# Kernel tuning notes

Hardware: AMD Instinct MI355X
Metric: run time of the kernel (lower is better)

## Reference

```python
import jax, jax.numpy as jnp
import numpy as np

B, R, C, OUT, IN = 256, 1152, 10, 16, 8


def setup_inputs() -> dict:
    key = jax.random.key(0)
    kx, kw = jax.random.split(key)
    x = jax.random.normal(kx, (B, R, IN), dtype=jnp.float32)
    W = jax.random.normal(kw, (R, C, OUT, IN), dtype=jnp.float32)
    return {"x": x, "W": W}


def _squash(s):
    # s: [B, C, OUT]
    mag_sq = jnp.sum(s * s, axis=-1, keepdims=True)
    mag = jnp.sqrt(mag_sq + 1e-8)
    return mag_sq / (1.0 + mag_sq) * (s / (mag + 1e-8))


def reference(x, W):
    # u_hat[b,r,c,o] = sum_i W[r,c,o,i] * x[b,r,i]  (no explicit W.repeat)
    u_hat = jnp.einsum('rcoi,bri->brco', W, x)
    b_ij = jnp.zeros((B, R, C), dtype=u_hat.dtype)
    v_j = None
    for it in range(3):
        c_ij = jax.nn.softmax(b_ij, axis=2)              # [B,R,C]
        s_j = jnp.einsum('brc,brco->bco', c_ij, u_hat)   # [B,C,OUT]
        v_j = _squash(s_j)                               # [B,C,OUT]
        if it < 2:
            b_ij = b_ij + jnp.einsum('brco,bco->brc', u_hat, v_j)
    return v_j
```

## Files before the change

kernel.cpp:

```cpp
#include <hip/hip_runtime.h>
#include <math.h>


typedef _Float16 h2 __attribute__((ext_vector_type(2)));
typedef _Float16 h4 __attribute__((ext_vector_type(4)));

#if __has_builtin(__builtin_amdgcn_fdot2)
#define FDOT2(a, b, c) __builtin_amdgcn_fdot2((a), (b), (c), false)
#else
static __device__ __forceinline__ float FDOT2(h2 a, h2 b, float c) {
    return c + (float)a.x * (float)b.x + (float)a.y * (float)b.y;
}
#endif

#if __has_builtin(__builtin_amdgcn_rcpf)
#define FRCP(x) __builtin_amdgcn_rcpf(x)
#else
#define FRCP(x) (1.0f / (x))
#endif

#define BCH2(u) __builtin_bit_cast(h2, (u))

template<int CTRL>
static __device__ __forceinline__ float dpp_xadd(float x) {
    const int t = __builtin_amdgcn_update_dpp(
        0, __builtin_bit_cast(int, x), CTRL, 0xF, 0xF, true);
    return x + __builtin_bit_cast(float, t);
}
static __device__ __forceinline__ float og_allsum(float l) {
    l = dpp_xadd<0xB1>(l);
    l = dpp_xadd<0x4E>(l);
    l = dpp_xadd<0x141>(l);
    return l;
}

namespace {
constexpr int Bdim = 256;
constexpr int Rdim = 1152;
constexpr int Cdim = 10;
constexpr int Odim = 16;
constexpr int Idim = 8;
constexpr int CO   = 160;

constexpr int Rpad  = 1280;
constexpr int RPC   = 10;
constexpr int NPAIR = 5;
constexpr int NSP   = 32;
constexpr int WROW  = Cdim * Odim * Idim;
}

__global__ __launch_bounds__(256)
void conv_wx(const float* __restrict__ W, const float* __restrict__ x,
             _Float16* __restrict__ W16, _Float16* __restrict__ X16)
{
    constexpr int NW4 = Rpad * WROW / 4;
    constexpr int NX4 = Rpad * Bdim * Idim / 4;
    const int i = blockIdx.x * 256 + threadIdx.x;
    if (i < NW4) {
        const int r = i / (WROW / 4);
        h4 o = { (_Float16)0.f, (_Float16)0.f, (_Float16)0.f, (_Float16)0.f };
        if (r < Rdim) {
            const float4 v = reinterpret_cast<const float4*>(W)[i];
            o = { (_Float16)v.x, (_Float16)v.y, (_Float16)v.z, (_Float16)v.w };
        }
        reinterpret_cast<h4*>(W16)[i] = o;
    } else if (i < NW4 + NX4) {
        const int j    = i - NW4;
        const int r    = j / (Bdim * 2);
        const int rem  = j - r * (Bdim * 2);
        const int b    = rem >> 1;
        const int half = rem & 1;
        h4 o = { (_Float16)0.f, (_Float16)0.f, (_Float16)0.f, (_Float16)0.f };
        if (r < Rdim) {
            const float4 v = reinterpret_cast<const float4*>(x)
                [((size_t)b * Rdim + r) * 2 + half];
            o = { (_Float16)v.x, (_Float16)v.y, (_Float16)v.z, (_Float16)v.w };
        }
        reinterpret_cast<h4*>(X16)[j] = o;
    }
}

__device__ __forceinline__ void stagepair(const _Float16* __restrict__ src,
                                          _Float16* dst, int lane)
{
#pragma unroll
    for (int k = 0; k < 5; ++k) {
        const _Float16* s = src + (size_t)(k * 64 + lane) * 8;
        _Float16* d = dst + k * 512;
        __builtin_amdgcn_global_load_lds((const __attribute__((address_space(1))) void*)s,
                                         (__attribute__((address_space(3))) void*)d,
                                         16, 0, 0);
    }
}

template<bool FIRST>
__global__ __launch_bounds__(256)
void caps_iter(const _Float16* __restrict__ X16, const _Float16* __restrict__ W16,
               const float* __restrict__ Vsum, float* __restrict__ s_part)
{
    __shared__ __align__(16) _Float16 Wst[4][3][2560];

    const int tid  = threadIdx.x;
    const int wv   = tid >> 6;
    const int lane = tid & 63;
    const int og   = lane & 7;
    const int bl   = lane >> 3;

    const int quad = blockIdx.x;
    const int bgrp = blockIdx.y;
    const int chunk = quad * 4 + wv;
    const int r0    = chunk * RPC;
    const int b0    = bgrp * 16 + bl;
    const int b1    = b0 + 8;

    float va0[Cdim], vb0[Cdim], va1[Cdim], vb1[Cdim];
    if constexpr (!FIRST) {
#pragma unroll
        for (int c = 0; c < Cdim; ++c) {
            const float2 p = *reinterpret_cast<const float2*>(
                Vsum + (size_t)b0 * CO + c * Odim + og * 2);
            va0[c] = p.x; vb0[c] = p.y;
            const float2 q = *reinterpret_cast<const float2*>(
                Vsum + (size_t)b1 * CO + c * Odim + og * 2);
            va1[c] = q.x; vb1[c] = q.y;
        }
    }

    float sA0[Cdim], sA1[Cdim], sB0[Cdim], sB1[Cdim];
#pragma unroll
    for (int c = 0; c < Cdim; ++c) { sA0[c]=0.f; sA1[c]=0.f; sB0[c]=0.f; sB1[c]=0.f; }

    const _Float16* Wr = W16 + (size_t)r0 * WROW;

    stagepair(Wr, &Wst[wv][0][0], lane);
    uint4 xc0, xc1, xc2, xc3;
    {
        const _Float16* xr = X16 + (size_t)r0 * (Bdim * Idim);
        xc0 = *reinterpret_cast<const uint4*>(xr + b0 * Idim);
        xc1 = *reinterpret_cast<const uint4*>(xr + b1 * Idim);
        xc2 = *reinterpret_cast<const uint4*>(xr + (Bdim * Idim) + b0 * Idim);
        xc3 = *reinterpret_cast<const uint4*>(xr + (Bdim * Idim) + b1 * Idim);
    }
    stagepair(Wr + 2 * WROW, &Wst[wv][1][0], lane);

    for (int p = 0; p < NPAIR; ++p) {
        if (p + 1 < NPAIR)
            asm volatile("s_waitcnt vmcnt(5)" ::: "memory");
        else
            asm volatile("s_waitcnt vmcnt(0)" ::: "memory");

        const _Float16* stcur = &Wst[wv][p % 3][0];

        uint4 xn0, xn1, xn2, xn3;
        if (p + 1 < NPAIR) {
            const _Float16* xr = X16 + (size_t)(r0 + (p + 1) * 2) * (Bdim * Idim);
            xn0 = *reinterpret_cast<const uint4*>(xr + b0 * Idim);
            xn1 = *reinterpret_cast<const uint4*>(xr + b1 * Idim);
            xn2 = *reinterpret_cast<const uint4*>(xr + (Bdim * Idim) + b0 * Idim);
            xn3 = *reinterpret_cast<const uint4*>(xr + (Bdim * Idim) + b1 * Idim);
        }
        if (p + 2 < NPAIR)
            stagepair(Wr + (size_t)(p + 2) * 2 * WROW, &Wst[wv][(p + 2) % 3][0], lane);

#pragma unroll
        for (int rl = 0; rl < 2; ++rl) {
            const uint4 xva = rl ? xc2 : xc0;
            const uint4 xvb = rl ? xc3 : xc1;
            const h2 a0 = BCH2(xva.x), a1 = BCH2(xva.y), a2 = BCH2(xva.z), a3 = BCH2(xva.w);
            const h2 e0 = BCH2(xvb.x), e1 = BCH2(xvb.y), e2 = BCH2(xvb.z), e3 = BCH2(xvb.w);

            const _Float16* wbase = stcur + rl * WROW + og * 16;
            float uA0[Cdim], uA1[Cdim], uB0[Cdim], uB1[Cdim];
#pragma unroll
            for (int g = 0; g < 2; ++g) {
                uint4 wreg[10];
#pragma unroll
                for (int c5 = 0; c5 < 5; ++c5) {
                    const uint4* wp = reinterpret_cast<const uint4*>(
                        wbase + (g * 5 + c5) * (Odim * Idim));
                    wreg[2 * c5]     = wp[0];
                    wreg[2 * c5 + 1] = wp[1];
                }
#pragma unroll
                for (int c5 = 0; c5 < 5; ++c5) {
                    const int c = g * 5 + c5;
                    const uint4 w0 = wreg[2 * c5], w1 = wreg[2 * c5 + 1];
                    float t;
                    t = FDOT2(BCH2(w0.x), a0, 0.f);  t = FDOT2(BCH2(w0.y), a1, t);
                    t = FDOT2(BCH2(w0.z), a2, t);    uA0[c] = FDOT2(BCH2(w0.w), a3, t);
                    t = FDOT2(BCH2(w1.x), a0, 0.f);  t = FDOT2(BCH2(w1.y), a1, t);
                    t = FDOT2(BCH2(w1.z), a2, t);    uA1[c] = FDOT2(BCH2(w1.w), a3, t);
                    t = FDOT2(BCH2(w0.x), e0, 0.f);  t = FDOT2(BCH2(w0.y), e1, t);
                    t = FDOT2(BCH2(w0.z), e2, t);    uB0[c] = FDOT2(BCH2(w0.w), e3, t);
                    t = FDOT2(BCH2(w1.x), e0, 0.f);  t = FDOT2(BCH2(w1.y), e1, t);
                    t = FDOT2(BCH2(w1.z), e2, t);    uB1[c] = FDOT2(BCH2(w1.w), e3, t);
                }
            }

            if constexpr (FIRST) {
#pragma unroll
                for (int c = 0; c < Cdim; ++c) {
                    sA0[c] += 0.1f * uA0[c];  sA1[c] += 0.1f * uA1[c];
                    sB0[c] += 0.1f * uB0[c];  sB1[c] += 0.1f * uB1[c];
                }
            } else {
                float eA[Cdim], eB[Cdim];
                float sumA = 0.f, sumB = 0.f;
#pragma unroll
                for (int c = 0; c < Cdim; ++c) {
                    float lA = uA0[c] * va0[c] + uA1[c] * vb0[c];
                    lA = og_allsum(lA);
                    eA[c] = __expf(lA);  sumA += eA[c];
                    float lB = uB0[c] * va1[c] + uB1[c] * vb1[c];
                    lB = og_allsum(lB);
                    eB[c] = __expf(lB);  sumB += eB[c];
                }
                const float rA = FRCP(sumA), rB = FRCP(sumB);
#pragma unroll
                for (int c = 0; c < Cdim; ++c) {
                    const float cwA = eA[c] * rA;
                    sA0[c] += cwA * uA0[c];  sA1[c] += cwA * uA1[c];
                    const float cwB = eB[c] * rB;
                    sB0[c] += cwB * uB0[c];  sB1[c] += cwB * uB1[c];
                }
            }
        }

        if (p + 1 < NPAIR) { xc0 = xn0; xc1 = xn1; xc2 = xn2; xc3 = xn3; }
    }

    __syncthreads();
    float* red = reinterpret_cast<float*>(&Wst[0][0][0]);
    {
        float* p0 = red + (wv * 16 + bl) * CO + og * 2;
        float* p1 = red + (wv * 16 + bl + 8) * CO + og * 2;
#pragma unroll
        for (int c = 0; c < Cdim; ++c) {
            *reinterpret_cast<float2*>(p0 + c * Odim) = make_float2(sA0[c], sA1[c]);
            *reinterpret_cast<float2*>(p1 + c * Odim) = make_float2(sB0[c], sB1[c]);
        }
    }
    __syncthreads();
#pragma unroll
    for (int k = 0; k < 10; ++k) {
        const int j = k * 256 + tid;
        const float t = red[j] + red[j + 2560] + red[j + 5120] + red[j + 7680];
        const int b2 = j / CO;
        const int co = j - b2 * CO;
        s_part[((size_t)quad * Bdim + bgrp * 16 + b2) * CO + co] = t;
    }
}

template<int MODE>
__global__ __launch_bounds__(256)
void caps_reduce(const float* __restrict__ s_part, float* __restrict__ Vsum,
                 float* __restrict__ out)
{
    const int idx = blockIdx.x * 256 + threadIdx.x;
    float s = 0.f;
#pragma unroll 8
    for (int k = 0; k < NSP; ++k) s += s_part[(size_t)k * (Bdim * CO) + idx];

    float ssq = s * s;
    ssq += __shfl_xor(ssq, 1);
    ssq += __shfl_xor(ssq, 2);
    ssq += __shfl_xor(ssq, 4);
    ssq += __shfl_xor(ssq, 8);

    const float mag = sqrtf(ssq + 1e-8f);
    const float v = ssq / (1.f + ssq) * s / (mag + 1e-8f);

    if constexpr (MODE == 2) out[idx] = v;
    else if constexpr (MODE == 1) Vsum[idx] += v;
    else Vsum[idx] = v;
}

extern "C" void kernel_launch(void* const* d_in, const int* in_sizes, int n_in,
                              void* d_out, int out_size, void* d_ws, size_t ws_size,
                              hipStream_t stream)
{
    const float* x = (const float*)d_in[0];
    const float* W = (const float*)d_in[1];
    float* out = (float*)d_out;

    float* s_part = (float*)d_ws;
    float* Vsum   = s_part + (size_t)NSP * Bdim * CO;
    _Float16* W16 = (_Float16*)(Vsum + Bdim * CO);
    _Float16* X16 = W16 + (size_t)Rpad * WROW;

    conv_wx<<<dim3(4160), dim3(256), 0, stream>>>(W, x, W16, X16);

    const dim3 gi(NSP, Bdim / 16);
    const dim3 bi(256);
    const dim3 gr((Bdim * CO) / 256);
    const dim3 br(256);

    caps_iter<true><<<gi, bi, 0, stream>>>(X16, W16, Vsum, s_part);
    caps_reduce<0><<<gr, br, 0, stream>>>(s_part, Vsum, out);
    caps_iter<false><<<gi, bi, 0, stream>>>(X16, W16, Vsum, s_part);
    caps_reduce<1><<<gr, br, 0, stream>>>(s_part, Vsum, out);
    caps_iter<false><<<gi, bi, 0, stream>>>(X16, W16, Vsum, s_part);
    caps_reduce<2><<<gr, br, 0, stream>>>(s_part, Vsum, out);
}
```

Baseline: 100.3 us.

## Read fp32 x directly in routing kernels and drop x fp16 conversion pass

Removes the pre-pass that converted and transposed x into an fp16 R-major buffer. The iteration kernels now load fp32 x straight from its original B-major layout and pack it to fp16 in registers, clamping the row index for padded chunks. The W staging pipeline goes from triple to double buffering with a uniform vmcnt wait, and the per-group W register batching becomes a simple per-class loop. This saves one conversion pass over x but triples x read traffic in fp32 and uses a less coalesced per-batch stride. The shallower prefetch may also expose more load latency.

```diff
diff --git a/kernel.cpp b/kernel.cpp
--- a/kernel.cpp
+++ b/kernel.cpp
@@ -12,6 +12,14 @@
     return c + (float)a.x * (float)b.x + (float)a.y * (float)b.y;
 }
 #endif
+
+static __device__ __forceinline__ h2 CVTPK(float a, float b) {
+#if __has_builtin(__builtin_amdgcn_cvt_pkrtz)
+    return __builtin_bit_cast(h2, __builtin_amdgcn_cvt_pkrtz(a, b));
+#else
+    h2 r; r.x = (_Float16)a; r.y = (_Float16)b; return r;
+#endif
+}
 
 #if __has_builtin(__builtin_amdgcn_rcpf)
 #define FRCP(x) __builtin_amdgcn_rcpf(x)
@@ -50,34 +58,16 @@
 }
 
 __global__ __launch_bounds__(256)
-void conv_wx(const float* __restrict__ W, const float* __restrict__ x,
-             _Float16* __restrict__ W16, _Float16* __restrict__ X16)
-{
-    constexpr int NW4 = Rpad * WROW / 4;
-    constexpr int NX4 = Rpad * Bdim * Idim / 4;
+void conv_w(const float* __restrict__ W, _Float16* __restrict__ W16)
+{
     const int i = blockIdx.x * 256 + threadIdx.x;
-    if (i < NW4) {
-        const int r = i / (WROW / 4);
-        h4 o = { (_Float16)0.f, (_Float16)0.f, (_Float16)0.f, (_Float16)0.f };
-        if (r < Rdim) {
-            const float4 v = reinterpret_cast<const float4*>(W)[i];
-            o = { (_Float16)v.x, (_Float16)v.y, (_Float16)v.z, (_Float16)v.w };
-        }
-        reinterpret_cast<h4*>(W16)[i] = o;
-    } else if (i < NW4 + NX4) {
-        const int j    = i - NW4;
-        const int r    = j / (Bdim * 2);
-        const int rem  = j - r * (Bdim * 2);
-        const int b    = rem >> 1;
-        const int half = rem & 1;
-        h4 o = { (_Float16)0.f, (_Float16)0.f, (_Float16)0.f, (_Float16)0.f };
-        if (r < Rdim) {
-            const float4 v = reinterpret_cast<const float4*>(x)
-                [((size_t)b * Rdim + r) * 2 + half];
-            o = { (_Float16)v.x, (_Float16)v.y, (_Float16)v.z, (_Float16)v.w };
-        }
-        reinterpret_cast<h4*>(X16)[j] = o;
-    }
+    const int r = i / (WROW / 4);
+    h4 o = { (_Float16)0.f, (_Float16)0.f, (_Float16)0.f, (_Float16)0.f };
+    if (r < Rdim) {
+        const float4 v = reinterpret_cast<const float4*>(W)[i];
+        o = { (_Float16)v.x, (_Float16)v.y, (_Float16)v.z, (_Float16)v.w };
+    }
+    reinterpret_cast<h4*>(W16)[i] = o;
 }
 
 __device__ __forceinline__ void stagepair(const _Float16* __restrict__ src,
@@ -95,10 +85,10 @@
 
 template<bool FIRST>
 __global__ __launch_bounds__(256)
-void caps_iter(const _Float16* __restrict__ X16, const _Float16* __restrict__ W16,
+void caps_iter(const float* __restrict__ xf, const _Float16* __restrict__ W16,
                const float* __restrict__ Vsum, float* __restrict__ s_part)
 {
-    __shared__ __align__(16) _Float16 Wst[4][3][2560];
+    __shared__ __align__(16) _Float16 Wst[4][2][2560];
 
     const int tid  = threadIdx.x;
     const int wv   = tid >> 6;
@@ -131,70 +121,71 @@
     for (int c = 0; c < Cdim; ++c) { sA0[c]=0.f; sA1[c]=0.f; sB0[c]=0.f; sB1[c]=0.f; }
 
     const _Float16* Wr = W16 + (size_t)r0 * WROW;
+    const float* xb0 = xf + (size_t)b0 * (Rdim * Idim);
+    const float* xb1 = xf + (size_t)b1 * (Rdim * Idim);
+
+    auto xoff = [&](int p) -> int {
+        int r = r0 + p * 2;
+        return (r > Rdim - 2 ? Rdim - 2 : r) * Idim;
+    };
 
     stagepair(Wr, &Wst[wv][0][0], lane);
-    uint4 xc0, xc1, xc2, xc3;
+    float4 xc[8];
     {
-        const _Float16* xr = X16 + (size_t)r0 * (Bdim * Idim);
-        xc0 = *reinterpret_cast<const uint4*>(xr + b0 * Idim);
-        xc1 = *reinterpret_cast<const uint4*>(xr + b1 * Idim);
-        xc2 = *reinterpret_cast<const uint4*>(xr + (Bdim * Idim) + b0 * Idim);
-        xc3 = *reinterpret_cast<const uint4*>(xr + (Bdim * Idim) + b1 * Idim);
-    }
-    stagepair(Wr + 2 * WROW, &Wst[wv][1][0], lane);
+        const int o0 = xoff(0);
+        xc[0] = *reinterpret_cast<const float4*>(xb0 + o0);
+        xc[1] = *reinterpret_cast<const float4*>(xb0 + o0 + 4);
+        xc[2] = *reinterpret_cast<const float4*>(xb0 + o0 + 8);
+        xc[3] = *reinterpret_cast<const float4*>(xb0 + o0 + 12);
+        xc[4] = *reinterpret_cast<const float4*>(xb1 + o0);
+        xc[5] = *reinterpret_cast<const float4*>(xb1 + o0 + 4);
+        xc[6] = *reinterpret_cast<const float4*>(xb1 + o0 + 8);
+        xc[7] = *reinterpret_cast<const float4*>(xb1 + o0 + 12);
+    }
 
     for (int p = 0; p < NPAIR; ++p) {
-        if (p + 1 < NPAIR)
-            asm volatile("s_waitcnt vmcnt(5)" ::: "memory");
-        else
-            asm volatile("s_waitcnt vmcnt(0)" ::: "memory");
-
-        const _Float16* stcur = &Wst[wv][p % 3][0];
-
-        uint4 xn0, xn1, xn2, xn3;
+        asm volatile("s_waitcnt vmcnt(8)" ::: "memory");
+
+        const _Float16* stcur = &Wst[wv][p & 1][0];
+
+        float4 xn[8];
         if (p + 1 < NPAIR) {
-            const _Float16* xr = X16 + (size_t)(r0 + (p + 1) * 2) * (Bdim * Idim);
-            xn0 = *reinterpret_cast<const uint4*>(xr + b0 * Idim);
-            xn1 = *reinterpret_cast<const uint4*>(xr + b1 * Idim);
-            xn2 = *reinterpret_cast<const uint4*>(xr + (Bdim * Idim) + b0 * Idim);
-            xn3 = *reinterpret_cast<const uint4*>(xr + (Bdim * Idim) + b1 * Idim);
-        }
-        if (p + 2 < NPAIR)
-            stagepair(Wr + (size_t)(p + 2) * 2 * WROW, &Wst[wv][(p + 2) % 3][0], lane);
+            stagepair(Wr + (size_t)(p + 1) * 2 * WROW, &Wst[wv][(p + 1) & 1][0], lane);
+            const int o1 = xoff(p + 1);
+            xn[0] = *reinterpret_cast<const float4*>(xb0 + o1);
+            xn[1] = *reinterpret_cast<const float4*>(xb0 + o1 + 4);
+            xn[2] = *reinterpret_cast<const float4*>(xb0 + o1 + 8);
+            xn[3] = *reinterpret_cast<const float4*>(xb0 + o1 + 12);
+            xn[4] = *reinterpret_cast<const float4*>(xb1 + o1);
+            xn[5] = *reinterpret_cast<const float4*>(xb1 + o1 + 4);
+            xn[6] = *reinterpret_cast<const float4*>(xb1 + o1 + 8);
+            xn[7] = *reinterpret_cast<const float4*>(xb1 + o1 + 12);
+        }
 
 #pragma unroll
         for (int rl = 0; rl < 2; ++rl) {
-            const uint4 xva = rl ? xc2 : xc0;
-            const uint4 xvb = rl ? xc3 : xc1;
-            const h2 a0 = BCH2(xva.x), a1 = BCH2(xva.y), a2 = BCH2(xva.z), a3 = BCH2(xva.w);
-            const h2 e0 = BCH2(xvb.x), e1 = BCH2(xvb.y), e2 = BCH2(xvb.z), e3 = BCH2(xvb.w);
+            const float4 pa0 = xc[rl * 2 + 0], pa1 = xc[rl * 2 + 1];
+            const float4 pb0 = xc[rl * 2 + 4], pb1 = xc[rl * 2 + 5];
+            const h2 a0 = CVTPK(pa0.x, pa0.y), a1 = CVTPK(pa0.z, pa0.w);
+            const h2 a2 = CVTPK(pa1.x, pa1.y), a3 = CVTPK(pa1.z, pa1.w);
+            const h2 e0 = CVTPK(pb0.x, pb0.y), e1 = CVTPK(pb0.z, pb0.w);
+            const h2 e2 = CVTPK(pb1.x, pb1.y), e3 = CVTPK(pb1.z, pb1.w);
 
             const _Float16* wbase = stcur + rl * WROW + og * 16;
             float uA0[Cdim], uA1[Cdim], uB0[Cdim], uB1[Cdim];
 #pragma unroll
-            for (int g = 0; g < 2; ++g) {
-                uint4 wreg[10];
-#pragma unroll
-                for (int c5 = 0; c5 < 5; ++c5) {
-                    const uint4* wp = reinterpret_cast<const uint4*>(
-                        wbase + (g * 5 + c5) * (Odim * Idim));
-                    wreg[2 * c5]     = wp[0];
-                    wreg[2 * c5 + 1] = wp[1];
-                }
-#pragma unroll
-                for (int c5 = 0; c5 < 5; ++c5) {
-                    const int c = g * 5 + c5;
-                    const uint4 w0 = wreg[2 * c5], w1 = wreg[2 * c5 + 1];
-                    float t;
-                    t = FDOT2(BCH2(w0.x), a0, 0.f);  t = FDOT2(BCH2(w0.y), a1, t);
-                    t = FDOT2(BCH2(w0.z), a2, t);    uA0[c] = FDOT2(BCH2(w0.w), a3, t);
-                    t = FDOT2(BCH2(w1.x), a0, 0.f);  t = FDOT2(BCH2(w1.y), a1, t);
-                    t = FDOT2(BCH2(w1.z), a2, t);    uA1[c] = FDOT2(BCH2(w1.w), a3, t);
-                    t = FDOT2(BCH2(w0.x), e0, 0.f);  t = FDOT2(BCH2(w0.y), e1, t);
-                    t = FDOT2(BCH2(w0.z), e2, t);    uB0[c] = FDOT2(BCH2(w0.w), e3, t);
-                    t = FDOT2(BCH2(w1.x), e0, 0.f);  t = FDOT2(BCH2(w1.y), e1, t);
-                    t = FDOT2(BCH2(w1.z), e2, t);    uB1[c] = FDOT2(BCH2(w1.w), e3, t);
-                }
+            for (int c = 0; c < Cdim; ++c) {
+                const uint4* wp = reinterpret_cast<const uint4*>(wbase + c * (Odim * Idim));
+                const uint4 w0 = wp[0], w1 = wp[1];
+                float t;
+                t = FDOT2(BCH2(w0.x), a0, 0.f);  t = FDOT2(BCH2(w0.y), a1, t);
+                t = FDOT2(BCH2(w0.z), a2, t);    uA0[c] = FDOT2(BCH2(w0.w), a3, t);
+                t = FDOT2(BCH2(w1.x), a0, 0.f);  t = FDOT2(BCH2(w1.y), a1, t);
+                t = FDOT2(BCH2(w1.z), a2, t);    uA1[c] = FDOT2(BCH2(w1.w), a3, t);
+                t = FDOT2(BCH2(w0.x), e0, 0.f);  t = FDOT2(BCH2(w0.y), e1, t);
+                t = FDOT2(BCH2(w0.z), e2, t);    uB0[c] = FDOT2(BCH2(w0.w), e3, t);
+                t = FDOT2(BCH2(w1.x), e0, 0.f);  t = FDOT2(BCH2(w1.y), e1, t);
+                t = FDOT2(BCH2(w1.z), e2, t);    uB1[c] = FDOT2(BCH2(w1.w), e3, t);
             }
 
             if constexpr (FIRST) {
@@ -226,7 +217,10 @@
             }
         }
 
-        if (p + 1 < NPAIR) { xc0 = xn0; xc1 = xn1; xc2 = xn2; xc3 = xn3; }
+        if (p + 1 < NPAIR) {
+#pragma unroll
+            for (int q = 0; q < 8; ++q) xc[q] = xn[q];
+        }
     }
 
     __syncthreads();
@@ -286,19 +280,18 @@
     float* s_part = (float*)d_ws;
     float* Vsum   = s_part + (size_t)NSP * Bdim * CO;
     _Float16* W16 = (_Float16*)(Vsum + Bdim * CO);
-    _Float16* X16 = W16 + (size_t)Rpad * WROW;
-
-    conv_wx<<<dim3(4160), dim3(256), 0, stream>>>(W, x, W16, X16);
+
+    conv_w<<<dim3(1600), dim3(256), 0, stream>>>(W, W16);
 
     const dim3 gi(NSP, Bdim / 16);
     const dim3 bi(256);
     const dim3 gr((Bdim * CO) / 256);
     const dim3 br(256);
 
-    caps_iter<true><<<gi, bi, 0, stream>>>(X16, W16, Vsum, s_part);
+    caps_iter<true><<<gi, bi, 0, stream>>>(x, W16, Vsum, s_part);
     caps_reduce<0><<<gr, br, 0, stream>>>(s_part, Vsum, out);
-    caps_iter<false><<<gi, bi, 0, stream>>>(X16, W16, Vsum, s_part);
+    caps_iter<false><<<gi, bi, 0, stream>>>(x, W16, Vsum, s_part);
     caps_reduce<1><<<gr, br, 0, stream>>>(s_part, Vsum, out);
-    caps_iter<false><<<gi, bi, 0, stream>>>(X16, W16, Vsum, s_part);
+    caps_iter<false><<<gi, bi, 0, stream>>>(x, W16, Vsum, s_part);
     caps_reduce<2><<<gr, br, 0, stream>>>(s_part, Vsum, out);
 }
```

Result: faster. 97.70 us (-2.6%).
